# Kernel tuning notes

Measured on AMD Instinct MI355X. Metric: run time of the kernel, lower is better.

Reference implementation:

```python
import jax, jax.numpy as jnp
import numpy as np

N = 50000      # nodes
E = 400000     # edges (before self loops)
F_IN = 128     # num_features
HID = 64       # hidden_dim
HEADS = 4
G = 64         # number of graphs in batch
NCLS = 2
NEG = 0.2      # leaky relu negative slope
BN_EPS = 1e-5


def setup_inputs() -> dict:
    key = jax.random.key(0)
    ks = jax.random.split(key, 32)
    rn = lambda k, shape, s=0.05: jax.random.normal(k, shape, jnp.float32) * s
    inp = {}
    inp["x"] = jax.random.normal(ks[0], (N, F_IN), jnp.float32)
    inp["edge_index"] = jax.random.randint(ks[1], (2, E), 0, N, dtype=jnp.int32)
    inp["batch"] = jnp.sort(jax.random.randint(ks[2], (N,), 0, G, dtype=jnp.int32))
    # layer 0 GATConv (concat=True) + pre projection
    inp["conv0_W"] = rn(ks[3], (F_IN, HEADS * HID))
    inp["conv0_att_src"] = rn(ks[4], (HEADS, HID))
    inp["conv0_att_dst"] = rn(ks[5], (HEADS, HID))
    inp["conv0_bias"] = jnp.zeros((HEADS * HID,), jnp.float32)
    inp["pre0_W"] = rn(ks[6], (HEADS * HID, HID))
    inp["pre0_b"] = jnp.zeros((HID,), jnp.float32)
    # layers 1..2 GATConv (concat=False), stacked
    inp["convs_W"] = rn(ks[7], (2, HID, HEADS * HID))
    inp["convs_att_src"] = rn(ks[8], (2, HEADS, HID))
    inp["convs_att_dst"] = rn(ks[9], (2, HEADS, HID))
    inp["convs_bias"] = jnp.zeros((2, HID), jnp.float32)
    # batch norms (eval mode: running stats)
    inp["bn_gamma"] = jnp.ones((3, HID), jnp.float32)
    inp["bn_beta"] = jnp.zeros((3, HID), jnp.float32)
    inp["bn_mean"] = rn(ks[10], (3, HID), 0.1)
    inp["bn_var"] = jax.random.uniform(ks[11], (3, HID), jnp.float32) + 0.5
    # JK projection, attention pooling, classifier
    inp["jump_W"] = rn(ks[12], (3 * HID, HID))
    inp["jump_b"] = jnp.zeros((HID,), jnp.float32)
    inp["att_W"] = rn(ks[13], (HID, 1))
    inp["att_b"] = jnp.zeros((1,), jnp.float32)
    inp["cls_W1"] = rn(ks[14], (HID, HID // 2))
    inp["cls_b1"] = jnp.zeros((HID // 2,), jnp.float32)
    inp["cls_W2"] = rn(ks[15], (HID // 2, NCLS))
    inp["cls_b2"] = jnp.zeros((NCLS,), jnp.float32)
    return inp


def _segment_softmax(logits, seg, num_segments):
    m = jax.ops.segment_max(logits, seg, num_segments=num_segments)
    e = jnp.exp(logits - m[seg])
    s = jax.ops.segment_sum(e, seg, num_segments=num_segments)
    return e / s[seg]


def _gat_conv(x, src, dst, W, a_src, a_dst, bias, concat):
    n = x.shape[0]
    H, C = a_src.shape
    xh = (x @ W).reshape(n, H, C)                         # [N, H, C]
    as_n = jnp.einsum('nhc,hc->nh', xh, a_src)            # [N, H]
    ad_n = jnp.einsum('nhc,hc->nh', xh, a_dst)            # [N, H]
    logits = jax.nn.leaky_relu(as_n[src] + ad_n[dst], NEG)  # [E', H]
    att = _segment_softmax(logits, dst, n)                # softmax over incoming edges
    out = jax.ops.segment_sum(xh[src] * att[:, :, None], dst, num_segments=n)
    out = out.reshape(n, H * C) if concat else out.mean(axis=1)
    return out + bias


def _bn(h, g, b, m, v):
    return (h - m) * jax.lax.rsqrt(v + BN_EPS) * g + b


def reference(x, edge_index, batch, conv0_W, conv0_att_src, conv0_att_dst,
              conv0_bias, pre0_W, pre0_b, convs_W, convs_att_src, convs_att_dst,
              convs_bias, bn_gamma, bn_beta, bn_mean, bn_var, jump_W, jump_b,
              att_W, att_b, cls_W1, cls_b1, cls_W2, cls_b2):
    n = x.shape[0]
    loops = jnp.arange(n, dtype=edge_index.dtype)
    src = jnp.concatenate([edge_index[0], loops])         # add_self_loops=True
    dst = jnp.concatenate([edge_index[1], loops])
    reps = []
    # layer 0: concat heads -> pre projection -> BN -> ELU (no residual: 128 != 64)
    h = _gat_conv(x, src, dst, conv0_W, conv0_att_src, conv0_att_dst, conv0_bias, True)
    h = h @ pre0_W + pre0_b
    h = jax.nn.elu(_bn(h, bn_gamma[0], bn_beta[0], bn_mean[0], bn_var[0]))
    reps.append(h)
    # layers 1..2: mean heads -> BN -> ELU -> residual
    for i in range(2):
        h_in = h
        h = _gat_conv(h, src, dst, convs_W[i], convs_att_src[i], convs_att_dst[i],
                      convs_bias[i], False)
        h = jax.nn.elu(_bn(h, bn_gamma[i + 1], bn_beta[i + 1], bn_mean[i + 1], bn_var[i + 1]))
        h = h + h_in
        reps.append(h)
    # jumping knowledge (cat)
    h = jnp.concatenate(reps, axis=-1) @ jump_W + jump_b  # [N, HID]
    # attentional global pooling
    a = _segment_softmax((h @ att_W + att_b)[:, 0], batch, G)  # [N]
    hg = jax.ops.segment_sum(h * a[:, None], batch, num_segments=G)  # [G, HID]
    # classifier
    return jax.nn.relu(hg @ cls_W1 + cls_b1) @ cls_W2 + cls_b2
```

## Files before the change

kernel.cpp:

```cpp
#include <hip/hip_runtime.h>
#include <hip/hip_bf16.h>
#include <math.h>

#define NEG 0.2f
#define BNEPS 1e-5f
#define NGRAPH 64
#define SCAN_CHUNK 2048
#define POOL_BLOCKS 256

typedef short bf16x8 __attribute__((ext_vector_type(8)));
typedef float f32x4  __attribute__((ext_vector_type(4)));

__device__ __forceinline__ float bf2f(unsigned short u) {
    return __uint_as_float(((unsigned)u) << 16);
}
__device__ __forceinline__ short f2bf(float f) {
    return (short)__bfloat16_as_ushort(__float2bfloat16(f));
}

__global__ __launch_bounds__(256)
void gemm_xh_mfma(const float* __restrict__ A, int lda,
                  const float* __restrict__ W, int Nc, int M, int K,
                  const float* __restrict__ att_s, const float* __restrict__ att_d,
                  float* __restrict__ as_out, float* __restrict__ ad_out,
                  unsigned short* __restrict__ Cbf)
{
    __shared__ short Wt[64 * 136];
    const int KP = K + 8;
    int tid  = threadIdx.x;
    int lane = tid & 63, wave = tid >> 6;
    int row0 = blockIdx.x * 64;
    int colb = blockIdx.y * 64;
    int c15 = lane & 15, q = lane >> 4;

    {
        int n = tid & 63;
        for (int k = tid >> 6; k < K; k += 4)
            Wt[n * KP + k] = f2bf(W[(size_t)k * Nc + colb + n]);
    }
    __syncthreads();

    int row = row0 + wave * 16 + c15;
    bool rok = row < M;
    const float* arow = A + (size_t)row * lda + q * 8;

    f32x4 acc[4];
    #pragma unroll
    for (int st = 0; st < 4; ++st) acc[st] = (f32x4){0.f, 0.f, 0.f, 0.f};

    for (int k0 = 0; k0 < K; k0 += 32) {
        bf16x8 av;
        if (rok) {
            float4 a0 = *(const float4*)(arow + k0);
            float4 a1 = *(const float4*)(arow + k0 + 4);
            av[0] = f2bf(a0.x); av[1] = f2bf(a0.y); av[2] = f2bf(a0.z); av[3] = f2bf(a0.w);
            av[4] = f2bf(a1.x); av[5] = f2bf(a1.y); av[6] = f2bf(a1.z); av[7] = f2bf(a1.w);
        } else {
            av = (bf16x8){0,0,0,0,0,0,0,0};
        }
        #pragma unroll
        for (int st = 0; st < 4; ++st) {
            bf16x8 bv = *(const bf16x8*)(Wt + (st * 16 + c15) * KP + k0 + q * 8);
            acc[st] = __builtin_amdgcn_mfma_f32_16x16x32_bf16(av, bv, acc[st], 0, 0, 0);
        }
    }

    #pragma unroll
    for (int r = 0; r < 4; ++r) {
        int orow = row0 + wave * 16 + q * 4 + r;
        if (orow >= M) continue;
        unsigned short* cb = Cbf + (size_t)orow * 256 + colb + c15;
        #pragma unroll
        for (int st = 0; st < 4; ++st)
            cb[st * 16] = (unsigned short)f2bf(acc[st][r]);
    }
    float sa[4], da[4];
    #pragma unroll
    for (int st = 0; st < 4; ++st) {
        sa[st] = att_s[colb + st * 16 + c15];
        da[st] = att_d[colb + st * 16 + c15];
    }
    #pragma unroll
    for (int r = 0; r < 4; ++r) {
        float ps = acc[0][r] * sa[0] + acc[1][r] * sa[1] + acc[2][r] * sa[2] + acc[3][r] * sa[3];
        float pd = acc[0][r] * da[0] + acc[1][r] * da[1] + acc[2][r] * da[2] + acc[3][r] * da[3];
        #pragma unroll
        for (int o = 1; o < 16; o <<= 1) {
            ps += __shfl_xor(ps, o);
            pd += __shfl_xor(pd, o);
        }
        int orow = row0 + wave * 16 + q * 4 + r;
        if (c15 == 0 && orow < M) {
            as_out[orow * 4 + blockIdx.y] = ps;
            ad_out[orow * 4 + blockIdx.y] = pd;
        }
    }
}

__global__ __launch_bounds__(256)
void gemm_n64_mfma(const void* __restrict__ Araw, int lda, int a_is_bf16,
                   const float* __restrict__ W, int M, int K,
                   const float* __restrict__ bias,
                   float* __restrict__ C, int ldc, int mode,
                   const float* __restrict__ bn_g, const float* __restrict__ bn_b,
                   const float* __restrict__ bn_m, const float* __restrict__ bn_v)
{
    __shared__ short Wt[64 * 264];
    const int KP = K + 8;
    int tid  = threadIdx.x;
    int lane = tid & 63, wave = tid >> 6;
    int row0 = blockIdx.x * 64;
    int c15 = lane & 15, q = lane >> 4;

    {
        int n = tid & 63;
        for (int k = tid >> 6; k < K; k += 4)
            Wt[n * KP + k] = f2bf(W[(size_t)k * 64 + n]);
    }
    __syncthreads();

    int row = row0 + wave * 16 + c15;
    bool rok = row < M;

    f32x4 acc[4];
    #pragma unroll
    for (int st = 0; st < 4; ++st) acc[st] = (f32x4){0.f, 0.f, 0.f, 0.f};

    for (int k0 = 0; k0 < K; k0 += 32) {
        bf16x8 av;
        if (rok) {
            if (a_is_bf16) {
                av = *(const bf16x8*)((const unsigned short*)Araw
                                      + (size_t)row * lda + k0 + q * 8);
            } else {
                const float* ap = (const float*)Araw + (size_t)row * lda + k0 + q * 8;
                float4 a0 = *(const float4*)ap;
                float4 a1 = *(const float4*)(ap + 4);
                av[0] = f2bf(a0.x); av[1] = f2bf(a0.y); av[2] = f2bf(a0.z); av[3] = f2bf(a0.w);
                av[4] = f2bf(a1.x); av[5] = f2bf(a1.y); av[6] = f2bf(a1.z); av[7] = f2bf(a1.w);
            }
        } else {
            av = (bf16x8){0,0,0,0,0,0,0,0};
        }
        #pragma unroll
        for (int st = 0; st < 4; ++st) {
            bf16x8 bv = *(const bf16x8*)(Wt + (st * 16 + c15) * KP + k0 + q * 8);
            acc[st] = __builtin_amdgcn_mfma_f32_16x16x32_bf16(av, bv, acc[st], 0, 0, 0);
        }
    }

    #pragma unroll
    for (int st = 0; st < 4; ++st) {
        int col = st * 16 + c15;
        float bs = bias ? bias[col] : 0.f;
        float sg = 1.f, sb = 0.f;
        if (mode == 1) {
            sg = bn_g[col] / sqrtf(bn_v[col] + BNEPS);
            sb = bn_b[col] - bn_m[col] * sg;
        }
        #pragma unroll
        for (int r = 0; r < 4; ++r) {
            int orow = row0 + wave * 16 + q * 4 + r;
            if (orow >= M) continue;
            float v = acc[st][r] + bs;
            if (mode == 1) {
                v = v * sg + sb;
                v = v > 0.f ? v : __expf(v) - 1.f;
            }
            C[(size_t)orow * ldc + col] = v;
        }
    }
}

__global__ __launch_bounds__(256)
void hist_kernel(const int* __restrict__ ei, int E, int N, int* __restrict__ counts)
{
    int e = blockIdx.x * blockDim.x + threadIdx.x;
    int Etot = E + N;
    if (e >= Etot) return;
    int d = (e < E) ? ei[E + e] : e - E;
    atomicAdd(&counts[d], 1);
}

__global__ __launch_bounds__(256)
void scan_phase1(const int* __restrict__ counts, int N, int* __restrict__ blocksum)
{
    __shared__ int wsum[4];
    int tid = threadIdx.x, lane = tid & 63, wave = tid >> 6;
    int base = blockIdx.x * SCAN_CHUNK;
    int s = 0;
    #pragma unroll
    for (int j = 0; j < SCAN_CHUNK / 256; ++j) {
        int idx = base + tid + j * 256;
        if (idx < N) s += counts[idx];
    }
    #pragma unroll
    for (int o = 32; o; o >>= 1) s += __shfl_xor(s, o);
    if (lane == 0) wsum[wave] = s;
    __syncthreads();
    if (tid == 0) blocksum[blockIdx.x] = wsum[0] + wsum[1] + wsum[2] + wsum[3];
}

__global__ void scan_phase2(const int* __restrict__ blocksum, int nb,
                            int* __restrict__ blockoff, int* __restrict__ rowptr, int N)
{
    int lane = threadIdx.x;
    int v = (lane < nb) ? blocksum[lane] : 0;
    int incl = v;
    #pragma unroll
    for (int o = 1; o < 64; o <<= 1) {
        int t = __shfl_up(incl, o);
        if (lane >= o) incl += t;
    }
    if (lane < nb) blockoff[lane + 1] = incl;
    if (lane == 0) blockoff[0] = 0;
    int total = __shfl(incl, nb - 1);
    if (lane == 0) rowptr[N] = total;
}

__global__ __launch_bounds__(256)
void scan_phase3(const int* __restrict__ counts, int N,
                 const int* __restrict__ blockoff,
                 int* __restrict__ rowptr, int* __restrict__ cursor)
{
    __shared__ int wsum[4];
    int tid = threadIdx.x, lane = tid & 63, wave = tid >> 6;
    int start = blockIdx.x * SCAN_CHUNK + tid * 8;
    int v[8];
    int s = 0;
    #pragma unroll
    for (int j = 0; j < 8; ++j) {
        v[j] = (start + j < N) ? counts[start + j] : 0;
        s += v[j];
    }
    int incl = s;
    #pragma unroll
    for (int o = 1; o < 64; o <<= 1) {
        int t = __shfl_up(incl, o);
        if (lane >= o) incl += t;
    }
    if (lane == 63) wsum[wave] = incl;
    __syncthreads();
    int woff = 0;
    #pragma unroll
    for (int w = 0; w < 4; ++w) if (w < wave) woff += wsum[w];
    int run = blockoff[blockIdx.x] + woff + incl - s;
    #pragma unroll
    for (int j = 0; j < 8; ++j) {
        int idx = start + j;
        if (idx < N) { rowptr[idx] = run; cursor[idx] = run; }
        run += v[j];
    }
}

__global__ __launch_bounds__(256)
void scatter_kernel(const int* __restrict__ ei, int E, int N,
                    int* __restrict__ cursor, int* __restrict__ csr_src)
{
    int e = blockIdx.x * blockDim.x + threadIdx.x;
    int Etot = E + N;
    if (e >= Etot) return;
    int s, d;
    if (e < E) { s = ei[e]; d = ei[E + e]; } else { s = d = e - E; }
    int pos = atomicAdd(&cursor[d], 1);
    csr_src[pos] = s;
}

__global__ __launch_bounds__(256)
void aggregate_kernel(const int* __restrict__ rowptr, const int* __restrict__ csr_src,
                      const float* __restrict__ as_n, const float* __restrict__ ad_n,
                      const unsigned short* __restrict__ xh,
                      const float* __restrict__ bias,
                      float* __restrict__ outp, int ldo,
                      int N, int mode,
                      const float* __restrict__ bn_g, const float* __restrict__ bn_b,
                      const float* __restrict__ bn_m, const float* __restrict__ bn_v,
                      const float* __restrict__ resid)
{
    int node = (blockIdx.x * blockDim.x + threadIdx.x) >> 6;
    int lane = threadIdx.x & 63;
    if (node >= N) return;
    int h = lane >> 4;
    int e0 = rowptr[node], e1 = rowptr[node + 1];

    float4 adv = ((const float4*)ad_n)[node];
    float adh = (h < 2) ? (h == 0 ? adv.x : adv.y) : (h == 2 ? adv.z : adv.w);

    float4 acc = make_float4(0.f, 0.f, 0.f, 0.f);
    float wsum = 0.f;
    int e = e0;
    for (; e + 3 < e1; e += 4) {
        int s0 = csr_src[e], s1 = csr_src[e + 1];
        int s2 = csr_src[e + 2], s3 = csr_src[e + 3];
        ushort4 xv0 = *(const ushort4*)(xh + (size_t)s0 * 256 + lane * 4);
        ushort4 xv1 = *(const ushort4*)(xh + (size_t)s1 * 256 + lane * 4);
        ushort4 xv2 = *(const ushort4*)(xh + (size_t)s2 * 256 + lane * 4);
        ushort4 xv3 = *(const ushort4*)(xh + (size_t)s3 * 256 + lane * 4);
        float a0 = as_n[s0 * 4 + h], a1 = as_n[s1 * 4 + h];
        float a2 = as_n[s2 * 4 + h], a3 = as_n[s3 * 4 + h];
        float l0 = a0 + adh, l1 = a1 + adh, l2 = a2 + adh, l3 = a3 + adh;
        l0 = fmaxf(l0, NEG * l0); l1 = fmaxf(l1, NEG * l1);
        l2 = fmaxf(l2, NEG * l2); l3 = fmaxf(l3, NEG * l3);
        float w0 = __expf(l0), w1 = __expf(l1), w2 = __expf(l2), w3 = __expf(l3);
        acc.x += w0 * bf2f(xv0.x); acc.y += w0 * bf2f(xv0.y);
        acc.z += w0 * bf2f(xv0.z); acc.w += w0 * bf2f(xv0.w);
        acc.x += w1 * bf2f(xv1.x); acc.y += w1 * bf2f(xv1.y);
        acc.z += w1 * bf2f(xv1.z); acc.w += w1 * bf2f(xv1.w);
        acc.x += w2 * bf2f(xv2.x); acc.y += w2 * bf2f(xv2.y);
        acc.z += w2 * bf2f(xv2.z); acc.w += w2 * bf2f(xv2.w);
        acc.x += w3 * bf2f(xv3.x); acc.y += w3 * bf2f(xv3.y);
        acc.z += w3 * bf2f(xv3.z); acc.w += w3 * bf2f(xv3.w);
        wsum += (w0 + w1) + (w2 + w3);
    }
    for (; e < e1; ++e) {
        int s0 = csr_src[e];
        float l0 = as_n[s0 * 4 + h] + adh;
        l0 = fmaxf(l0, NEG * l0);
        float w0 = __expf(l0);
        ushort4 xv0 = *(const ushort4*)(xh + (size_t)s0 * 256 + lane * 4);
        acc.x += w0 * bf2f(xv0.x); acc.y += w0 * bf2f(xv0.y);
        acc.z += w0 * bf2f(xv0.z); acc.w += w0 * bf2f(xv0.w);
        wsum += w0;
    }
    float rw = 1.f / wsum;
    acc.x *= rw; acc.y *= rw; acc.z *= rw; acc.w *= rw;

    if (mode == 0) {
        float4 bs = *(const float4*)(bias + lane * 4);
        ushort4 pk;
        pk.x = (unsigned short)f2bf(acc.x + bs.x);
        pk.y = (unsigned short)f2bf(acc.y + bs.y);
        pk.z = (unsigned short)f2bf(acc.z + bs.z);
        pk.w = (unsigned short)f2bf(acc.w + bs.w);
        *(ushort4*)((unsigned short*)outp + (size_t)node * 256 + lane * 4) = pk;
    } else {
        #pragma unroll
        for (int off = 16; off <= 32; off <<= 1) {
            acc.x += __shfl_xor(acc.x, off);
            acc.y += __shfl_xor(acc.y, off);
            acc.z += __shfl_xor(acc.z, off);
            acc.w += __shfl_xor(acc.w, off);
        }
        if (lane < 16) {
            int cin = lane * 4;
            float4 bs = *(const float4*)(bias + cin);
            float4 g = *(const float4*)(bn_g + cin);
            float4 b = *(const float4*)(bn_b + cin);
            float4 m = *(const float4*)(bn_m + cin);
            float4 vv = *(const float4*)(bn_v + cin);
            float4 rs = *(const float4*)(resid + (size_t)node * ldo + cin);
            float o[4] = {acc.x, acc.y, acc.z, acc.w};
            float bb[4] = {bs.x, bs.y, bs.z, bs.w};
            float gg[4] = {g.x, g.y, g.z, g.w};
            float be[4] = {b.x, b.y, b.z, b.w};
            float mm[4] = {m.x, m.y, m.z, m.w};
            float va[4] = {vv.x, vv.y, vv.z, vv.w};
            float rr[4] = {rs.x, rs.y, rs.z, rs.w};
            float4 res;
            float* rp = &res.x;
            #pragma unroll
            for (int j = 0; j < 4; ++j) {
                float v = 0.25f * o[j] + bb[j];
                float sg = gg[j] / sqrtf(va[j] + BNEPS);
                v = (v - mm[j]) * sg + be[j];
                v = v > 0.f ? v : __expf(v) - 1.f;
                rp[j] = v + rr[j];
            }
            *(float4*)(outp + (size_t)node * ldo + cin) = res;
        }
    }
}

__global__ __launch_bounds__(256)
void att_logit_kernel(const float* __restrict__ hjk, const float* __restrict__ attW,
                      const float* __restrict__ attb, float* __restrict__ wout, int N)
{
    int wid  = (blockIdx.x * blockDim.x + threadIdx.x) >> 6;
    int lane = threadIdx.x & 63;
    if (wid >= N) return;
    float v = hjk[(size_t)wid * 64 + lane] * attW[lane];
    #pragma unroll
    for (int off = 32; off; off >>= 1) v += __shfl_xor(v, off);
    if (lane == 0) wout[wid] = __expf(v + attb[0]);
}

__global__ void gstart_kernel(const int* __restrict__ batch, int N, int* __restrict__ gstart)
{
    int t = threadIdx.x;
    if (t > NGRAPH) return;
    int lo = 0, hi = N;
    while (lo < hi) {
        int mid = (lo + hi) >> 1;
        if (batch[mid] < t) lo = mid + 1; else hi = mid;
    }
    gstart[t] = lo;
}

__global__ __launch_bounds__(256)
void pool_partial(const float* __restrict__ hjk, const float* __restrict__ w,
                  const int* __restrict__ batch, const int* __restrict__ gstart,
                  float* __restrict__ hg_acc, float* __restrict__ wsum_acc, int N)
{
    __shared__ float red[256];
    __shared__ float wred[4];
    int tid = threadIdx.x;
    int c = tid & 63, q = tid >> 6;
    int slab = (N + POOL_BLOCKS - 1) / POOL_BLOCKS;
    int n0 = blockIdx.x * slab;
    int n1 = n0 + slab; if (n1 > N) n1 = N;
    if (n0 >= n1) return;
    int g0 = batch[n0], g1 = batch[n1 - 1];

    for (int g = g0; g <= g1; ++g) {
        int s = gstart[g];     if (s < n0) s = n0;
        int e = gstart[g + 1]; if (e > n1) e = n1;
        float acc = 0.f, ws = 0.f;
        for (int n = s + q; n < e; n += 4) {
            float wn = w[n];
            acc += wn * hjk[(size_t)n * 64 + c];
            if (c == 0) ws += wn;
        }
        red[tid] = acc;
        if (c == 0) wred[q] = ws;
        __syncthreads();
        if (q == 0) {
            float v = red[c] + red[64 + c] + red[128 + c] + red[192 + c];
            if (v != 0.f) atomicAdd(&hg_acc[g * 64 + c], v);
            if (c == 0) {
                float t = wred[0] + wred[1] + wred[2] + wred[3];
                if (t != 0.f) atomicAdd(&wsum_acc[g], t);
            }
        }
        __syncthreads();
    }
}

__global__ void cls_kernel(const float* __restrict__ hg_acc,
                           const float* __restrict__ wsum_acc,
                           const float* __restrict__ W1, const float* __restrict__ b1,
                           const float* __restrict__ W2, const float* __restrict__ b2,
                           float* __restrict__ out)
{
    int g = blockIdx.x, t = threadIdx.x;
    __shared__ float z[32];
    __shared__ float h[64];
    float wsum = wsum_acc[g];
    float rw = (wsum > 0.f) ? 1.f / wsum : 0.f;
    h[t] = hg_acc[g * 64 + t] * rw;
    h[t + 32] = hg_acc[g * 64 + t + 32] * rw;
    __syncthreads();
    float acc = b1[t];
    for (int k = 0; k < 64; ++k) acc += h[k] * W1[k * 32 + t];
    z[t] = fmaxf(acc, 0.f);
    __syncthreads();
    if (t < 2) {
        float o = b2[t];
        for (int j = 0; j < 32; ++j) o += z[j] * W2[j * 2 + t];
        out[g * 2 + t] = o;
    }
}

extern "C" void kernel_launch(void* const* d_in, const int* in_sizes, int n_in,
                              void* d_out, int out_size, void* d_ws, size_t ws_size,
                              hipStream_t stream)
{
    const float* x        = (const float*)d_in[0];
    const int*   ei       = (const int*)d_in[1];
    const int*   batch    = (const int*)d_in[2];
    const float* conv0_W  = (const float*)d_in[3];
    const float* conv0_as = (const float*)d_in[4];
    const float* conv0_ad = (const float*)d_in[5];
    const float* conv0_b  = (const float*)d_in[6];
    const float* pre0_W   = (const float*)d_in[7];
    const float* pre0_b   = (const float*)d_in[8];
    const float* convs_W  = (const float*)d_in[9];
    const float* convs_as = (const float*)d_in[10];
    const float* convs_ad = (const float*)d_in[11];
    const float* convs_b  = (const float*)d_in[12];
    const float* bn_g     = (const float*)d_in[13];
    const float* bn_b     = (const float*)d_in[14];
    const float* bn_m     = (const float*)d_in[15];
    const float* bn_v     = (const float*)d_in[16];
    const float* jump_W   = (const float*)d_in[17];
    const float* jump_b   = (const float*)d_in[18];
    const float* att_W    = (const float*)d_in[19];
    const float* att_b    = (const float*)d_in[20];
    const float* cls_W1   = (const float*)d_in[21];
    const float* cls_b1   = (const float*)d_in[22];
    const float* cls_W2   = (const float*)d_in[23];
    const float* cls_b2   = (const float*)d_in[24];
    float* out = (float*)d_out;

    const int N = in_sizes[0] / 128;
    const int E = in_sizes[1] / 2;
    const int Etot = E + N;
    const int nb = (N + SCAN_CHUNK - 1) / SCAN_CHUNK;

    float* ws      = (float*)d_ws;
    unsigned short* xh_bf   = (unsigned short*)ws;
    unsigned short* h256_bf = xh_bf + (size_t)N * 256;
    float* repsAll = (float*)(h256_bf + (size_t)N * 256);
    float* as_n    = repsAll + (size_t)N * 192;
    float* ad_n    = as_n + (size_t)N * 4;
    float* hjk     = ad_n + (size_t)N * 4;
    float* hg_acc  = hjk + (size_t)N * 64;
    float* wsum_acc= hg_acc + NGRAPH * 64;
    int*   rowptr  = (int*)(wsum_acc + NGRAPH);
    int*   cursor  = rowptr + (N + 1);
    int*   counts  = cursor + N;
    int*   csr_src = counts + N;
    int*   gstart  = csr_src + Etot;
    int*   blocksum = gstart + (NGRAPH + 1);
    int*   blockoff = blocksum + 64;
    float* wbuf    = as_n;

    dim3 blk(256);
    int node_wave_blocks = (N + 3) / 4;
    int edge_blocks      = (Etot + 255) / 256;

    hipMemsetAsync(counts, 0, (size_t)N * sizeof(int), stream);
    hist_kernel<<<edge_blocks, blk, 0, stream>>>(ei, E, N, counts);
    scan_phase1<<<nb, blk, 0, stream>>>(counts, N, blocksum);
    scan_phase2<<<1, 64, 0, stream>>>(blocksum, nb, blockoff, rowptr, N);
    scan_phase3<<<nb, blk, 0, stream>>>(counts, N, blockoff, rowptr, cursor);
    scatter_kernel<<<edge_blocks, blk, 0, stream>>>(ei, E, N, cursor, csr_src);

    {
        dim3 g1((N + 63) / 64, 4);
        gemm_xh_mfma<<<g1, blk, 0, stream>>>(x, 128, conv0_W, 256, N, 128,
                                             conv0_as, conv0_ad, as_n, ad_n, xh_bf);
        aggregate_kernel<<<node_wave_blocks, blk, 0, stream>>>(
            rowptr, csr_src, as_n, ad_n, xh_bf, conv0_b, (float*)h256_bf, 256, N, 0,
            nullptr, nullptr, nullptr, nullptr, nullptr);
        dim3 g2((N + 63) / 64, 1);
        gemm_n64_mfma<<<g2, blk, 0, stream>>>(h256_bf, 256, 1, pre0_W, N, 256,
                                              pre0_b, repsAll, 192, 1,
                                              bn_g, bn_b, bn_m, bn_v);
    }

    for (int i = 0; i < 2; ++i) {
        dim3 g1((N + 63) / 64, 4);
        gemm_xh_mfma<<<g1, blk, 0, stream>>>(repsAll + i * 64, 192,
                                             convs_W + (size_t)i * 64 * 256, 256, N, 64,
                                             convs_as + i * 256, convs_ad + i * 256,
                                             as_n, ad_n, xh_bf);
        aggregate_kernel<<<node_wave_blocks, blk, 0, stream>>>(
            rowptr, csr_src, as_n, ad_n, xh_bf, convs_b + i * 64,
            repsAll + (i + 1) * 64, 192, N, 1,
            bn_g + (i + 1) * 64, bn_b + (i + 1) * 64,
            bn_m + (i + 1) * 64, bn_v + (i + 1) * 64,
            repsAll + i * 64);
    }

    {
        dim3 g2((N + 63) / 64, 1);
        gemm_n64_mfma<<<g2, blk, 0, stream>>>(repsAll, 192, 0, jump_W, N, 192,
                                              jump_b, hjk, 64, 0,
                                              nullptr, nullptr, nullptr, nullptr);
    }

    att_logit_kernel<<<node_wave_blocks, blk, 0, stream>>>(hjk, att_W, att_b, wbuf, N);
    gstart_kernel<<<1, 128, 0, stream>>>(batch, N, gstart);
    hipMemsetAsync(hg_acc, 0, (NGRAPH * 64 + NGRAPH) * sizeof(float), stream);
    pool_partial<<<POOL_BLOCKS, blk, 0, stream>>>(hjk, wbuf, batch, gstart,
                                                  hg_acc, wsum_acc, N);
    cls_kernel<<<NGRAPH, 32, 0, stream>>>(hg_acc, wsum_acc, cls_W1, cls_b1,
                                          cls_W2, cls_b2, out);
}
```

Baseline: 429.7 us.

## Fuse attention logit into JK GEMM and split aggregation edges across half-waves

The attention-pooling logit and exp are now computed in the epilogue of the jumping-knowledge GEMM, which removes a separate kernel launch and a re-read of hjk. The aggregation kernel is also restructured: each half-wave handles alternate edges and loads 8 bf16 values per lane, and the halves are combined with cross-lane shuffles at the end. This doubles the edge-level parallelism and widens the loads per node, at the cost of more registers and extra shuffle reductions.

```diff
diff --git a/kernel.cpp b/kernel.cpp
--- a/kernel.cpp
+++ b/kernel.cpp
@@ -10,6 +10,7 @@
 
 typedef short bf16x8 __attribute__((ext_vector_type(8)));
 typedef float f32x4  __attribute__((ext_vector_type(4)));
+typedef unsigned short ushort8 __attribute__((ext_vector_type(8)));
 
 __device__ __forceinline__ float bf2f(unsigned short u) {
     return __uint_as_float(((unsigned)u) << 16);
@@ -103,7 +104,9 @@
                    const float* __restrict__ bias,
                    float* __restrict__ C, int ldc, int mode,
                    const float* __restrict__ bn_g, const float* __restrict__ bn_b,
-                   const float* __restrict__ bn_m, const float* __restrict__ bn_v)
+                   const float* __restrict__ bn_m, const float* __restrict__ bn_v,
+                   const float* __restrict__ attW, const float* __restrict__ attb,
+                   float* __restrict__ wout)
 {
     __shared__ short Wt[64 * 264];
     const int KP = K + 8;
@@ -167,7 +170,24 @@
                 v = v * sg + sb;
                 v = v > 0.f ? v : __expf(v) - 1.f;
             }
+            acc[st][r] = v;
             C[(size_t)orow * ldc + col] = v;
+        }
+    }
+
+    if (wout) {
+        float sa[4];
+        #pragma unroll
+        for (int st = 0; st < 4; ++st) sa[st] = attW[st * 16 + c15];
+        float ab = attb[0];
+        #pragma unroll
+        for (int r = 0; r < 4; ++r) {
+            float ps = acc[0][r] * sa[0] + acc[1][r] * sa[1]
+                     + acc[2][r] * sa[2] + acc[3][r] * sa[3];
+            #pragma unroll
+            for (int o = 1; o < 16; o <<= 1) ps += __shfl_xor(ps, o);
+            int orow = row0 + wave * 16 + q * 4 + r;
+            if (c15 == 0 && orow < M) wout[orow] = __expf(ps + ab);
         }
     }
 }
@@ -280,108 +300,82 @@
     int node = (blockIdx.x * blockDim.x + threadIdx.x) >> 6;
     int lane = threadIdx.x & 63;
     if (node >= N) return;
-    int h = lane >> 4;
+    int half = lane >> 5;
+    int li   = lane & 31;
+    int h    = li >> 3;
+
     int e0 = rowptr[node], e1 = rowptr[node + 1];
-
-    float4 adv = ((const float4*)ad_n)[node];
-    float adh = (h < 2) ? (h == 0 ? adv.x : adv.y) : (h == 2 ? adv.z : adv.w);
-
-    float4 acc = make_float4(0.f, 0.f, 0.f, 0.f);
+    float adh = ad_n[node * 4 + h];
+
+    float acc[8] = {0.f,0.f,0.f,0.f,0.f,0.f,0.f,0.f};
     float wsum = 0.f;
-    int e = e0;
-    for (; e + 3 < e1; e += 4) {
-        int s0 = csr_src[e], s1 = csr_src[e + 1];
-        int s2 = csr_src[e + 2], s3 = csr_src[e + 3];
-        ushort4 xv0 = *(const ushort4*)(xh + (size_t)s0 * 256 + lane * 4);
-        ushort4 xv1 = *(const ushort4*)(xh + (size_t)s1 * 256 + lane * 4);
-        ushort4 xv2 = *(const ushort4*)(xh + (size_t)s2 * 256 + lane * 4);
-        ushort4 xv3 = *(const ushort4*)(xh + (size_t)s3 * 256 + lane * 4);
-        float a0 = as_n[s0 * 4 + h], a1 = as_n[s1 * 4 + h];
-        float a2 = as_n[s2 * 4 + h], a3 = as_n[s3 * 4 + h];
-        float l0 = a0 + adh, l1 = a1 + adh, l2 = a2 + adh, l3 = a3 + adh;
-        l0 = fmaxf(l0, NEG * l0); l1 = fmaxf(l1, NEG * l1);
-        l2 = fmaxf(l2, NEG * l2); l3 = fmaxf(l3, NEG * l3);
-        float w0 = __expf(l0), w1 = __expf(l1), w2 = __expf(l2), w3 = __expf(l3);
-        acc.x += w0 * bf2f(xv0.x); acc.y += w0 * bf2f(xv0.y);
-        acc.z += w0 * bf2f(xv0.z); acc.w += w0 * bf2f(xv0.w);
-        acc.x += w1 * bf2f(xv1.x); acc.y += w1 * bf2f(xv1.y);
-        acc.z += w1 * bf2f(xv1.z); acc.w += w1 * bf2f(xv1.w);
-        acc.x += w2 * bf2f(xv2.x); acc.y += w2 * bf2f(xv2.y);
-        acc.z += w2 * bf2f(xv2.z); acc.w += w2 * bf2f(xv2.w);
-        acc.x += w3 * bf2f(xv3.x); acc.y += w3 * bf2f(xv3.y);
-        acc.z += w3 * bf2f(xv3.z); acc.w += w3 * bf2f(xv3.w);
-        wsum += (w0 + w1) + (w2 + w3);
-    }
-    for (; e < e1; ++e) {
-        int s0 = csr_src[e];
-        float l0 = as_n[s0 * 4 + h] + adh;
-        l0 = fmaxf(l0, NEG * l0);
-        float w0 = __expf(l0);
-        ushort4 xv0 = *(const ushort4*)(xh + (size_t)s0 * 256 + lane * 4);
-        acc.x += w0 * bf2f(xv0.x); acc.y += w0 * bf2f(xv0.y);
-        acc.z += w0 * bf2f(xv0.z); acc.w += w0 * bf2f(xv0.w);
-        wsum += w0;
-    }
+
+    int e = e0 + half;
+    for (; e + 2 < e1; e += 4) {
+        int sA = csr_src[e], sB = csr_src[e + 2];
+        ushort8 xvA = *(const ushort8*)(xh + (size_t)sA * 256 + li * 8);
+        ushort8 xvB = *(const ushort8*)(xh + (size_t)sB * 256 + li * 8);
+        float aA = as_n[sA * 4 + h];
+        float aB = as_n[sB * 4 + h];
+        float lA = aA + adh; lA = fmaxf(lA, NEG * lA);
+        float lB = aB + adh; lB = fmaxf(lB, NEG * lB);
+        float wA = __expf(lA), wB = __expf(lB);
+        #pragma unroll
+        for (int j = 0; j < 8; ++j) acc[j] += wA * bf2f(xvA[j]);
+        #pragma unroll
+        for (int j = 0; j < 8; ++j) acc[j] += wB * bf2f(xvB[j]);
+        wsum += wA + wB;
+    }
+    for (; e < e1; e += 2) {
+        int sA = csr_src[e];
+        ushort8 xvA = *(const ushort8*)(xh + (size_t)sA * 256 + li * 8);
+        float lA = as_n[sA * 4 + h] + adh;
+        lA = fmaxf(lA, NEG * lA);
+        float wA = __expf(lA);
+        #pragma unroll
+        for (int j = 0; j < 8; ++j) acc[j] += wA * bf2f(xvA[j]);
+        wsum += wA;
+    }
+
+    #pragma unroll
+    for (int j = 0; j < 8; ++j) acc[j] += __shfl_xor(acc[j], 32);
+    wsum += __shfl_xor(wsum, 32);
     float rw = 1.f / wsum;
-    acc.x *= rw; acc.y *= rw; acc.z *= rw; acc.w *= rw;
 
     if (mode == 0) {
-        float4 bs = *(const float4*)(bias + lane * 4);
-        ushort4 pk;
-        pk.x = (unsigned short)f2bf(acc.x + bs.x);
-        pk.y = (unsigned short)f2bf(acc.y + bs.y);
-        pk.z = (unsigned short)f2bf(acc.z + bs.z);
-        pk.w = (unsigned short)f2bf(acc.w + bs.w);
-        *(ushort4*)((unsigned short*)outp + (size_t)node * 256 + lane * 4) = pk;
+        if (half == 0) {
+            int c0 = li * 8;
+            ushort8 pk;
+            #pragma unroll
+            for (int j = 0; j < 8; ++j)
+                pk[j] = (unsigned short)f2bf(acc[j] * rw + bias[c0 + j]);
+            *(ushort8*)((unsigned short*)outp + (size_t)node * 256 + c0) = pk;
+        }
     } else {
         #pragma unroll
-        for (int off = 16; off <= 32; off <<= 1) {
-            acc.x += __shfl_xor(acc.x, off);
-            acc.y += __shfl_xor(acc.y, off);
-            acc.z += __shfl_xor(acc.z, off);
-            acc.w += __shfl_xor(acc.w, off);
-        }
-        if (lane < 16) {
-            int cin = lane * 4;
-            float4 bs = *(const float4*)(bias + cin);
-            float4 g = *(const float4*)(bn_g + cin);
-            float4 b = *(const float4*)(bn_b + cin);
-            float4 m = *(const float4*)(bn_m + cin);
-            float4 vv = *(const float4*)(bn_v + cin);
-            float4 rs = *(const float4*)(resid + (size_t)node * ldo + cin);
-            float o[4] = {acc.x, acc.y, acc.z, acc.w};
-            float bb[4] = {bs.x, bs.y, bs.z, bs.w};
-            float gg[4] = {g.x, g.y, g.z, g.w};
-            float be[4] = {b.x, b.y, b.z, b.w};
-            float mm[4] = {m.x, m.y, m.z, m.w};
-            float va[4] = {vv.x, vv.y, vv.z, vv.w};
-            float rr[4] = {rs.x, rs.y, rs.z, rs.w};
-            float4 res;
-            float* rp = &res.x;
+        for (int j = 0; j < 8; ++j) acc[j] *= rw;
+        #pragma unroll
+        for (int j = 0; j < 8; ++j) {
+            acc[j] += __shfl_xor(acc[j], 8);
+            acc[j] += __shfl_xor(acc[j], 16);
+        }
+        if (lane < 8) {
+            int cin = lane * 8;
+            float res[8];
             #pragma unroll
-            for (int j = 0; j < 4; ++j) {
-                float v = 0.25f * o[j] + bb[j];
-                float sg = gg[j] / sqrtf(va[j] + BNEPS);
-                v = (v - mm[j]) * sg + be[j];
+            for (int j = 0; j < 8; ++j) {
+                int c = cin + j;
+                float v = 0.25f * acc[j] + bias[c];
+                float sg = bn_g[c] / sqrtf(bn_v[c] + BNEPS);
+                v = (v - bn_m[c]) * sg + bn_b[c];
                 v = v > 0.f ? v : __expf(v) - 1.f;
-                rp[j] = v + rr[j];
+                res[j] = v + resid[(size_t)node * ldo + c];
             }
-            *(float4*)(outp + (size_t)node * ldo + cin) = res;
-        }
-    }
-}
-
-__global__ __launch_bounds__(256)
-void att_logit_kernel(const float* __restrict__ hjk, const float* __restrict__ attW,
-                      const float* __restrict__ attb, float* __restrict__ wout, int N)
-{
-    int wid  = (blockIdx.x * blockDim.x + threadIdx.x) >> 6;
-    int lane = threadIdx.x & 63;
-    if (wid >= N) return;
-    float v = hjk[(size_t)wid * 64 + lane] * attW[lane];
-    #pragma unroll
-    for (int off = 32; off; off >>= 1) v += __shfl_xor(v, off);
-    if (lane == 0) wout[wid] = __expf(v + attb[0]);
+            float* op = outp + (size_t)node * ldo + cin;
+            *(float4*)op       = make_float4(res[0], res[1], res[2], res[3]);
+            *(float4*)(op + 4) = make_float4(res[4], res[5], res[6], res[7]);
+        }
+    }
 }
 
 __global__ void gstart_kernel(const int* __restrict__ batch, int N, int* __restrict__ gstart)
@@ -535,7 +529,8 @@
         dim3 g2((N + 63) / 64, 1);
         gemm_n64_mfma<<<g2, blk, 0, stream>>>(h256_bf, 256, 1, pre0_W, N, 256,
                                               pre0_b, repsAll, 192, 1,
-                                              bn_g, bn_b, bn_m, bn_v);
+                                              bn_g, bn_b, bn_m, bn_v,
+                                              nullptr, nullptr, nullptr);
     }
 
     for (int i = 0; i < 2; ++i) {
@@ -556,10 +551,10 @@
         dim3 g2((N + 63) / 64, 1);
         gemm_n64_mfma<<<g2, blk, 0, stream>>>(repsAll, 192, 0, jump_W, N, 192,
                                               jump_b, hjk, 64, 0,
-                                              nullptr, nullptr, nullptr, nullptr);
-    }
-
-    att_logit_kernel<<<node_wave_blocks, blk, 0, stream>>>(hjk, att_W, att_b, wbuf, N);
+                                              nullptr, nullptr, nullptr, nullptr,
+                                              att_W, att_b, wbuf);
+    }
+
     gstart_kernel<<<1, 128, 0, stream>>>(batch, N, gstart);
     hipMemsetAsync(hg_acc, 0, (NGRAPH * 64 + NGRAPH) * sizeof(float), stream);
     pool_partial<<<POOL_BLOCKS, blk, 0, stream>>>(hjk, wbuf, batch, gstart,
```

Measured after the change: 428.7 us. Within noise of the previous version (-0.2%).

## Precompute per-edge attention weights in CSR order and fuse pooling logits into GEMM

Applied to the files above, without the earlier changes.

The scatter kernel now records each edge's CSR position, and a new per-edge kernel computes the exp(leaky_relu) attention weights for all four heads once per layer, writing them in CSR order. The aggregation kernel reads these weights instead of recomputing them from per-node gathered scores, so each weight is computed once rather than redundantly across the 16 lanes of a head. Separately, the attention-pooling logit is fused into the jump-projection GEMM epilogue, removing the standalone att_logit kernel and its reread of hjk. The cost is an extra kernel launch per layer and an additional E×4 float buffer that is written and then read back.

```diff
diff --git a/kernel.cpp b/kernel.cpp
--- a/kernel.cpp
+++ b/kernel.cpp
@@ -103,7 +103,9 @@
                    const float* __restrict__ bias,
                    float* __restrict__ C, int ldc, int mode,
                    const float* __restrict__ bn_g, const float* __restrict__ bn_b,
-                   const float* __restrict__ bn_m, const float* __restrict__ bn_v)
+                   const float* __restrict__ bn_m, const float* __restrict__ bn_v,
+                   const float* __restrict__ attW, const float* __restrict__ attb,
+                   float* __restrict__ wout)
 {
     __shared__ short Wt[64 * 264];
     const int KP = K + 8;
@@ -167,7 +169,24 @@
                 v = v * sg + sb;
                 v = v > 0.f ? v : __expf(v) - 1.f;
             }
+            acc[st][r] = v;
             C[(size_t)orow * ldc + col] = v;
+        }
+    }
+
+    if (wout) {
+        float sa[4];
+        #pragma unroll
+        for (int st = 0; st < 4; ++st) sa[st] = attW[st * 16 + c15];
+        float ab = attb[0];
+        #pragma unroll
+        for (int r = 0; r < 4; ++r) {
+            float ps = acc[0][r] * sa[0] + acc[1][r] * sa[1]
+                     + acc[2][r] * sa[2] + acc[3][r] * sa[3];
+            #pragma unroll
+            for (int o = 1; o < 16; o <<= 1) ps += __shfl_xor(ps, o);
+            int orow = row0 + wave * 16 + q * 4 + r;
+            if (c15 == 0 && orow < M) wout[orow] = __expf(ps + ab);
         }
     }
 }
@@ -255,7 +274,8 @@
 
 __global__ __launch_bounds__(256)
 void scatter_kernel(const int* __restrict__ ei, int E, int N,
-                    int* __restrict__ cursor, int* __restrict__ csr_src)
+                    int* __restrict__ cursor, int* __restrict__ csr_src,
+                    int* __restrict__ epos)
 {
     int e = blockIdx.x * blockDim.x + threadIdx.x;
     int Etot = E + N;
@@ -264,11 +284,33 @@
     if (e < E) { s = ei[e]; d = ei[E + e]; } else { s = d = e - E; }
     int pos = atomicAdd(&cursor[d], 1);
     csr_src[pos] = s;
+    epos[e] = pos;
+}
+
+__global__ __launch_bounds__(256)
+void edge_weight_kernel(const int* __restrict__ ei, int E, int N,
+                        const int* __restrict__ epos,
+                        const float* __restrict__ as_n, const float* __restrict__ ad_n,
+                        float* __restrict__ w_csr)
+{
+    int e = blockIdx.x * blockDim.x + threadIdx.x;
+    int Etot = E + N;
+    if (e >= Etot) return;
+    int s, d;
+    if (e < E) { s = ei[e]; d = ei[E + e]; } else { s = d = e - E; }
+    float4 asv = ((const float4*)as_n)[s];
+    float4 adv = ((const float4*)ad_n)[d];
+    float l0 = asv.x + adv.x; l0 = fmaxf(l0, NEG * l0);
+    float l1 = asv.y + adv.y; l1 = fmaxf(l1, NEG * l1);
+    float l2 = asv.z + adv.z; l2 = fmaxf(l2, NEG * l2);
+    float l3 = asv.w + adv.w; l3 = fmaxf(l3, NEG * l3);
+    ((float4*)w_csr)[epos[e]] =
+        make_float4(__expf(l0), __expf(l1), __expf(l2), __expf(l3));
 }
 
 __global__ __launch_bounds__(256)
 void aggregate_kernel(const int* __restrict__ rowptr, const int* __restrict__ csr_src,
-                      const float* __restrict__ as_n, const float* __restrict__ ad_n,
+                      const float* __restrict__ w_csr,
                       const unsigned short* __restrict__ xh,
                       const float* __restrict__ bias,
                       float* __restrict__ outp, int ldo,
@@ -283,25 +325,20 @@
     int h = lane >> 4;
     int e0 = rowptr[node], e1 = rowptr[node + 1];
 
-    float4 adv = ((const float4*)ad_n)[node];
-    float adh = (h < 2) ? (h == 0 ? adv.x : adv.y) : (h == 2 ? adv.z : adv.w);
-
     float4 acc = make_float4(0.f, 0.f, 0.f, 0.f);
     float wsum = 0.f;
     int e = e0;
     for (; e + 3 < e1; e += 4) {
         int s0 = csr_src[e], s1 = csr_src[e + 1];
         int s2 = csr_src[e + 2], s3 = csr_src[e + 3];
+        float w0 = w_csr[(e    ) * 4 + h];
+        float w1 = w_csr[(e + 1) * 4 + h];
+        float w2 = w_csr[(e + 2) * 4 + h];
+        float w3 = w_csr[(e + 3) * 4 + h];
         ushort4 xv0 = *(const ushort4*)(xh + (size_t)s0 * 256 + lane * 4);
         ushort4 xv1 = *(const ushort4*)(xh + (size_t)s1 * 256 + lane * 4);
         ushort4 xv2 = *(const ushort4*)(xh + (size_t)s2 * 256 + lane * 4);
         ushort4 xv3 = *(const ushort4*)(xh + (size_t)s3 * 256 + lane * 4);
-        float a0 = as_n[s0 * 4 + h], a1 = as_n[s1 * 4 + h];
-        float a2 = as_n[s2 * 4 + h], a3 = as_n[s3 * 4 + h];
-        float l0 = a0 + adh, l1 = a1 + adh, l2 = a2 + adh, l3 = a3 + adh;
-        l0 = fmaxf(l0, NEG * l0); l1 = fmaxf(l1, NEG * l1);
-        l2 = fmaxf(l2, NEG * l2); l3 = fmaxf(l3, NEG * l3);
-        float w0 = __expf(l0), w1 = __expf(l1), w2 = __expf(l2), w3 = __expf(l3);
         acc.x += w0 * bf2f(xv0.x); acc.y += w0 * bf2f(xv0.y);
         acc.z += w0 * bf2f(xv0.z); acc.w += w0 * bf2f(xv0.w);
         acc.x += w1 * bf2f(xv1.x); acc.y += w1 * bf2f(xv1.y);
@@ -314,9 +351,7 @@
     }
     for (; e < e1; ++e) {
         int s0 = csr_src[e];
-        float l0 = as_n[s0 * 4 + h] + adh;
-        l0 = fmaxf(l0, NEG * l0);
-        float w0 = __expf(l0);
+        float w0 = w_csr[e * 4 + h];
         ushort4 xv0 = *(const ushort4*)(xh + (size_t)s0 * 256 + lane * 4);
         acc.x += w0 * bf2f(xv0.x); acc.y += w0 * bf2f(xv0.y);
         acc.z += w0 * bf2f(xv0.z); acc.w += w0 * bf2f(xv0.w);
@@ -371,19 +406,6 @@
     }
 }
 
-__global__ __launch_bounds__(256)
-void att_logit_kernel(const float* __restrict__ hjk, const float* __restrict__ attW,
-                      const float* __restrict__ attb, float* __restrict__ wout, int N)
-{
-    int wid  = (blockIdx.x * blockDim.x + threadIdx.x) >> 6;
-    int lane = threadIdx.x & 63;
-    if (wid >= N) return;
-    float v = hjk[(size_t)wid * 64 + lane] * attW[lane];
-    #pragma unroll
-    for (int off = 32; off; off >>= 1) v += __shfl_xor(v, off);
-    if (lane == 0) wout[wid] = __expf(v + attb[0]);
-}
-
 __global__ void gstart_kernel(const int* __restrict__ batch, int N, int* __restrict__ gstart)
 {
     int t = threadIdx.x;
@@ -503,13 +525,15 @@
     float* as_n    = repsAll + (size_t)N * 192;
     float* ad_n    = as_n + (size_t)N * 4;
     float* hjk     = ad_n + (size_t)N * 4;
-    float* hg_acc  = hjk + (size_t)N * 64;
+    float* w_csr   = hjk + (size_t)N * 64;
+    float* hg_acc  = w_csr + (size_t)Etot * 4;
     float* wsum_acc= hg_acc + NGRAPH * 64;
     int*   rowptr  = (int*)(wsum_acc + NGRAPH);
     int*   cursor  = rowptr + (N + 1);
     int*   counts  = cursor + N;
     int*   csr_src = counts + N;
-    int*   gstart  = csr_src + Etot;
+    int*   epos    = csr_src + Etot;
+    int*   gstart  = epos + Etot;
     int*   blocksum = gstart + (NGRAPH + 1);
     int*   blockoff = blocksum + 64;
     float* wbuf    = as_n;
@@ -523,19 +547,22 @@
     scan_phase1<<<nb, blk, 0, stream>>>(counts, N, blocksum);
     scan_phase2<<<1, 64, 0, stream>>>(blocksum, nb, blockoff, rowptr, N);
     scan_phase3<<<nb, blk, 0, stream>>>(counts, N, blockoff, rowptr, cursor);
-    scatter_kernel<<<edge_blocks, blk, 0, stream>>>(ei, E, N, cursor, csr_src);
+    scatter_kernel<<<edge_blocks, blk, 0, stream>>>(ei, E, N, cursor, csr_src, epos);
 
     {
         dim3 g1((N + 63) / 64, 4);
         gemm_xh_mfma<<<g1, blk, 0, stream>>>(x, 128, conv0_W, 256, N, 128,
                                              conv0_as, conv0_ad, as_n, ad_n, xh_bf);
+        edge_weight_kernel<<<edge_blocks, blk, 0, stream>>>(ei, E, N, epos,
+                                                            as_n, ad_n, w_csr);
         aggregate_kernel<<<node_wave_blocks, blk, 0, stream>>>(
-            rowptr, csr_src, as_n, ad_n, xh_bf, conv0_b, (float*)h256_bf, 256, N, 0,
+            rowptr, csr_src, w_csr, xh_bf, conv0_b, (float*)h256_bf, 256, N, 0,
             nullptr, nullptr, nullptr, nullptr, nullptr);
         dim3 g2((N + 63) / 64, 1);
         gemm_n64_mfma<<<g2, blk, 0, stream>>>(h256_bf, 256, 1, pre0_W, N, 256,
                                               pre0_b, repsAll, 192, 1,
-                                              bn_g, bn_b, bn_m, bn_v);
+                                              bn_g, bn_b, bn_m, bn_v,
+                                              nullptr, nullptr, nullptr);
     }
 
     for (int i = 0; i < 2; ++i) {
@@ -544,8 +571,10 @@
                                              convs_W + (size_t)i * 64 * 256, 256, N, 64,
                                              convs_as + i * 256, convs_ad + i * 256,
                                              as_n, ad_n, xh_bf);
+        edge_weight_kernel<<<edge_blocks, blk, 0, stream>>>(ei, E, N, epos,
+                                                            as_n, ad_n, w_csr);
         aggregate_kernel<<<node_wave_blocks, blk, 0, stream>>>(
-            rowptr, csr_src, as_n, ad_n, xh_bf, convs_b + i * 64,
+            rowptr, csr_src, w_csr, xh_bf, convs_b + i * 64,
             repsAll + (i + 1) * 64, 192, N, 1,
             bn_g + (i + 1) * 64, bn_b + (i + 1) * 64,
             bn_m + (i + 1) * 64, bn_v + (i + 1) * 64,
@@ -556,10 +585,10 @@
         dim3 g2((N + 63) / 64, 1);
         gemm_n64_mfma<<<g2, blk, 0, stream>>>(repsAll, 192, 0, jump_W, N, 192,
                                               jump_b, hjk, 64, 0,
-                                              nullptr, nullptr, nullptr, nullptr);
-    }
-
-    att_logit_kernel<<<node_wave_blocks, blk, 0, stream>>>(hjk, att_W, att_b, wbuf, N);
+                                              nullptr, nullptr, nullptr, nullptr,
+                                              att_W, att_b, wbuf);
+    }
+
     gstart_kernel<<<1, 128, 0, stream>>>(batch, N, gstart);
     hipMemsetAsync(hg_acc, 0, (NGRAPH * 64 + NGRAPH) * sizeof(float), stream);
     pool_partial<<<POOL_BLOCKS, blk, 0, stream>>>(hjk, wbuf, batch, gstart,
```

Result: slower. 442.8 us (+3.1%).
